# Kernel optimization log

Measured on AMD Instinct MI355X. Metric: run time of the kernel, lower is better.

The kernel has to match this reference:

```python
import jax, jax.numpy as jnp
import numpy as np

INPUT, HIDDEN, CLASSES = 4096, 4096, 1000


def setup_inputs() -> dict:
    key = jax.random.key(0)
    kx, kw1, kb1, kw2, kb2 = jax.random.split(key, 5)
    return {
        "x": jax.random.normal(kx, (8192, INPUT), dtype=jnp.float32),
        "fc1_weight": jax.random.normal(kw1, (HIDDEN, INPUT), dtype=jnp.float32),
        "fc1_bias": jax.random.normal(kb1, (HIDDEN,), dtype=jnp.float32),
        "fc2_weight": jax.random.normal(kw2, (CLASSES, HIDDEN), dtype=jnp.float32),
        "fc2_bias": jax.random.normal(kb2, (CLASSES,), dtype=jnp.float32),
    }


def reference(x, fc1_weight, fc1_bias, fc2_weight, fc2_bias):
    # x: [B, INPUT] (module flattens; already flat here)
    hidden = jnp.einsum("bi,hi->bh", x, fc1_weight) + fc1_bias  # [B, H]
    activated = jax.nn.relu(hidden)
    logits = jnp.einsum("bh,ch->bc", activated, fc2_weight) + fc2_bias  # [B, C]
    return jax.nn.softmax(logits, axis=-1)
```

## Files before the change

kernel.cpp:

```cpp
#include <hip/hip_runtime.h>
#include <hip/hip_fp16.h>
#include <stdint.h>

typedef __attribute__((ext_vector_type(8)))  _Float16 f16x8;
typedef __attribute__((ext_vector_type(4)))  _Float16 f16x4;
typedef __attribute__((ext_vector_type(4)))  float    f32x4;
typedef __attribute__((ext_vector_type(16))) float    f32x16;

__device__ __forceinline__ void split4(const f32x4 v, f16x4 &h, f16x4 &l) {
    #pragma unroll
    for (int i = 0; i < 4; ++i) {
        float a = v[i];
        _Float16 hh = (_Float16)a;
        h[i] = hh;
        l[i] = (_Float16)(a - (float)hh);
    }
}

__global__ __launch_bounds__(256)
void split_rows(const float* __restrict__ src, _Float16* __restrict__ h,
                _Float16* __restrict__ l, int srcRows, long long total4)
{
    const long long stride = (long long)gridDim.x * blockDim.x;
    for (long long i = (long long)blockIdx.x * blockDim.x + threadIdx.x; i < total4; i += stride) {
        const long long e = i << 2;
        const int row = (int)(e >> 12);
        f16x4 hv = {}, lv = {};
        if (row < srcRows) {
            f32x4 v = *(const f32x4*)(src + e);
            split4(v, hv, lv);
        }
        *(f16x4*)(h + e) = hv;
        *(f16x4*)(l + e) = lv;
    }
}


#define BARRIER() __builtin_amdgcn_s_barrier()
#define SB0()     __builtin_amdgcn_sched_barrier(0)
#define MFMA32    __builtin_amdgcn_mfma_f32_32x32x16_f16

template<int N> __device__ __forceinline__ void VMCNT() {
    asm volatile("s_waitcnt vmcnt(%0)" :: "n"(N) : "memory");
    __builtin_amdgcn_sched_barrier(0);
}

__device__ __forceinline__ void gload16(const _Float16* g, _Float16* l) {
    __builtin_amdgcn_global_load_lds(
        (const __attribute__((address_space(1))) void*)g,
        (__attribute__((address_space(3))) void*)l, 16, 0, 0);
}

template<int MI, bool SPLITOUT, bool CHUNKSWZ>
__global__ __launch_bounds__(512, 2)
void gemm3_v6(const _Float16* __restrict__ Agh, const _Float16* __restrict__ Agl,
              const _Float16* __restrict__ Bgh, const _Float16* __restrict__ Bgl,
              const float* __restrict__ bias,
              _Float16* __restrict__ Oh, _Float16* __restrict__ Ol,
              float* __restrict__ Of, int ldo, int Nstore,
              int K, int nBM)
{
    extern __shared__ _Float16 lds[];
    constexpr int WROWS = MI * 16;
    constexpr int BM    = MI * 32;
    constexpr int MB    = MI / 2;
    constexpr int MBH   = MB / 2;
    constexpr int CHA   = MI * 2;
    constexpr int PW    = (2*CHA + 32) / 8;
    constexpr int H2    = CHA / 8;
    constexpr int H1    = PW - H2;
    constexpr int ALO   = CHA * 512;
    constexpr int BHO   = 2 * CHA * 512;
    constexpr int BUFS  = 2*CHA*512 + 16384;

    const int tid  = threadIdx.x;
    const int lane = tid & 63;
    const int wave = tid >> 6;
    const int wm  = wave >> 2;
    const int wn  = wave & 3;
    const int l31 = lane & 31;
    const int lhi = lane >> 5;

    int bm, bn;
    const int orig = blockIdx.x;
    if (CHUNKSWZ) {
        bm = ((orig & 7) << 2) | ((orig >> 3) & 3);
        bn = orig >> 5;
    } else {
        const int cpx  = gridDim.x >> 3;
        const int swzb = (orig & 7) * cpx + (orig >> 3);
        bm = swzb % nBM;
        bn = swzb / nBM;
    }
    const int m0 = bm * BM;
    const int n0 = bn * 256;

    const _Float16* gptr[8];
    int loff[8];
    #pragma unroll
    for (int i = 0; i < PW; ++i) {
        int p, q;
        if (i < H2 || i >= H1) {
            const bool hi = (i >= H1);
            const int  s  = hi ? (i - H1) : i;
            const int  j  = wave * H2 + s;
            p = j / (CHA / 2);
            const int v   = j % (CHA / 2);
            const int wmq = v / (MI / 2);
            const int wi  = v % (MI / 2);
            q = wmq * MI + (hi ? MI / 2 : 0) + wi;
        } else {
            q = (i - H2) + (wave & 3) * 4;
            p = 2 + (wave >> 2);
        }
        const int row = q*16 + (lane >> 2);
        const int gc  = (lane & 3) ^ ((row >> 1) & 3);
        const _Float16* plane = (p == 0) ? Agh : (p == 1) ? Agl : (p == 2) ? Bgh : Bgl;
        const size_t grow = (size_t)((p < 2) ? m0 : n0) + row;
        gptr[i] = plane + grow * (size_t)K + gc * 8;
        loff[i] = ((p < 2) ? p * ALO : BHO + (p - 2) * 8192) + q * 512;
    }

    const int kxor = (l31 >> 1) & 3;
    int aoff[MB][2], boff[2][2];
    #pragma unroll
    for (int mb = 0; mb < MB; ++mb)
        #pragma unroll
        for (int kh = 0; kh < 2; ++kh)
            aoff[mb][kh] = (wm*WROWS + mb*32 + l31)*32 + ((kh*2 + lhi) ^ kxor)*8;
    #pragma unroll
    for (int nb = 0; nb < 2; ++nb)
        #pragma unroll
        for (int kh = 0; kh < 2; ++kh)
            boff[nb][kh] = BHO + (wn*64 + nb*32 + l31)*32 + ((kh*2 + lhi) ^ kxor)*8;

    f32x16 acc[MB][2] = {};

    #pragma unroll
    for (int i = 0; i < PW; ++i) { gload16(gptr[i], &lds[loff[i]]); gptr[i] += 32; }
    VMCNT<H2>(); BARRIER(); SB0();

#define DO_HALF(MBB, IB, IE)                                                  \
    do {                                                                      \
        _Pragma("unroll")                                                     \
        for (int i = (IB); i < (IE); ++i) {                                   \
            gload16(gptr[i], &lds[nbuf + loff[i]]); gptr[i] += 32;            \
        }                                                                     \
        SB0();                                                                \
        _Pragma("unroll")                                                     \
        for (int kh = 0; kh < 2; ++kh) {                                      \
            f16x8 ah[MBH], al[MBH];                                           \
            _Pragma("unroll")                                                 \
            for (int m2 = 0; m2 < MBH; ++m2) {                                \
                ah[m2] = *(const f16x8*)&lds[bb + aoff[(MBB) + m2][kh]];      \
                al[m2] = *(const f16x8*)&lds[bb + ALO + aoff[(MBB) + m2][kh]];\
            }                                                                 \
            __builtin_amdgcn_s_setprio(1);                                    \
            _Pragma("unroll")                                                 \
            for (int m2 = 0; m2 < MBH; ++m2) {                                \
                _Pragma("unroll")                                             \
                for (int n2 = 0; n2 < 2; ++n2) {                              \
                    acc[(MBB)+m2][n2] = MFMA32(ah[m2], bh[n2][kh], acc[(MBB)+m2][n2], 0, 0, 0); \
                    acc[(MBB)+m2][n2] = MFMA32(ah[m2], bl[n2][kh], acc[(MBB)+m2][n2], 0, 0, 0); \
                    acc[(MBB)+m2][n2] = MFMA32(al[m2], bh[n2][kh], acc[(MBB)+m2][n2], 0, 0, 0); \
                }                                                             \
            }                                                                 \
            __builtin_amdgcn_s_setprio(0);                                    \
        }                                                                     \
    } while (0)

    const int NT = K >> 5;
    int bb = 0;
    for (int t = 0; t < NT - 1; ++t) {
        const int nbuf = BUFS - bb;
        f16x8 bh[2][2], bl[2][2];
        #pragma unroll
        for (int nb = 0; nb < 2; ++nb)
            #pragma unroll
            for (int kh = 0; kh < 2; ++kh) {
                bh[nb][kh] = *(const f16x8*)&lds[bb + boff[nb][kh]];
                bl[nb][kh] = *(const f16x8*)&lds[bb + 8192 + boff[nb][kh]];
            }
        DO_HALF(0, 0, H1);
        VMCNT<H1>(); BARRIER(); SB0();
        DO_HALF(MBH, H1, PW);
        VMCNT<H2>(); BARRIER(); SB0();
        bb = nbuf;
    }
    {
        const int nbuf = bb;
        f16x8 bh[2][2], bl[2][2];
        #pragma unroll
        for (int nb = 0; nb < 2; ++nb)
            #pragma unroll
            for (int kh = 0; kh < 2; ++kh) {
                bh[nb][kh] = *(const f16x8*)&lds[bb + boff[nb][kh]];
                bl[nb][kh] = *(const f16x8*)&lds[bb + 8192 + boff[nb][kh]];
            }
        DO_HALF(0, 0, 0);
        VMCNT<0>(); BARRIER(); SB0();
        DO_HALF(MBH, 0, 0);
        (void)nbuf;
    }
#undef DO_HALF

    #pragma unroll
    for (int nb = 0; nb < 2; ++nb) {
        const int n = n0 + wn*64 + nb*32 + l31;
        if (!SPLITOUT && n >= Nstore) continue;
        const float bv = bias[n];
        #pragma unroll
        for (int mb = 0; mb < MB; ++mb) {
            #pragma unroll
            for (int r = 0; r < 16; ++r) {
                const int m = m0 + wm*WROWS + mb*32 + (r & 3) + 8*(r >> 2) + 4*lhi;
                float v = acc[mb][nb][r] + bv;
                if (SPLITOUT) {
                    v = fmaxf(v, 0.f);
                    const _Float16 hh = (_Float16)v;
                    Oh[(size_t)m * ldo + n] = hh;
                    Ol[(size_t)m * ldo + n] = (_Float16)(v - (float)hh);
                } else {
                    Of[(size_t)m * ldo + n] = v;
                }
            }
        }
    }
}

#define TILE_M 128
#define TILE_N 128
#define TILE_K 32
#define LDSK   40

template<bool RELU, bool NGUARD>
__global__ __launch_bounds__(256, 2)
void gemm_split3(const float* __restrict__ A, const float* __restrict__ B,
                 const float* __restrict__ bias, float* __restrict__ C,
                 int K, int ldc, int Nreal)
{
    __shared__ _Float16 Ah[TILE_M][LDSK];
    __shared__ _Float16 Al[TILE_M][LDSK];
    __shared__ _Float16 Bh[TILE_N][LDSK];
    __shared__ _Float16 Bl[TILE_N][LDSK];

    const int tid  = threadIdx.x;
    const int lane = tid & 63;
    const int wave = tid >> 6;
    const int wr   = wave >> 1;
    const int wc   = wave & 1;
    const int m0   = blockIdx.x * TILE_M;
    const int n0   = blockIdx.y * TILE_N;
    const int srow = tid >> 3;
    const int scol = (tid & 7) << 2;
    const int fr = lane & 15;
    const int fg = lane >> 4;

    f32x4 acc[4][4] = {};

    for (int kt = 0; kt < K; kt += TILE_K) {
        __syncthreads();
        #pragma unroll
        for (int p = 0; p < 4; ++p) {
            const int row = srow + p * 32;
            f32x4 v = *(const f32x4*)(A + (size_t)(m0 + row) * K + kt + scol);
            f16x4 hv, lv;
            split4(v, hv, lv);
            *(f16x4*)&Ah[row][scol] = hv;
            *(f16x4*)&Al[row][scol] = lv;
        }
        #pragma unroll
        for (int p = 0; p < 4; ++p) {
            const int row = srow + p * 32;
            f32x4 v = {0.f, 0.f, 0.f, 0.f};
            if (!NGUARD || (n0 + row) < Nreal)
                v = *(const f32x4*)(B + (size_t)(n0 + row) * K + kt + scol);
            f16x4 hv, lv;
            split4(v, hv, lv);
            *(f16x4*)&Bh[row][scol] = hv;
            *(f16x4*)&Bl[row][scol] = lv;
        }
        __syncthreads();

        f16x8 ah[4], al[4];
        #pragma unroll
        for (int mi = 0; mi < 4; ++mi) {
            const int r = wr * 64 + mi * 16 + fr;
            ah[mi] = *(const f16x8*)&Ah[r][fg * 8];
            al[mi] = *(const f16x8*)&Al[r][fg * 8];
        }
        #pragma unroll
        for (int ni = 0; ni < 4; ++ni) {
            const int r = wc * 64 + ni * 16 + fr;
            const f16x8 bh = *(const f16x8*)&Bh[r][fg * 8];
            const f16x8 bl = *(const f16x8*)&Bl[r][fg * 8];
            #pragma unroll
            for (int mi = 0; mi < 4; ++mi) {
                acc[mi][ni] = __builtin_amdgcn_mfma_f32_16x16x32_f16(ah[mi], bh, acc[mi][ni], 0, 0, 0);
                acc[mi][ni] = __builtin_amdgcn_mfma_f32_16x16x32_f16(ah[mi], bl, acc[mi][ni], 0, 0, 0);
                acc[mi][ni] = __builtin_amdgcn_mfma_f32_16x16x32_f16(al[mi], bh, acc[mi][ni], 0, 0, 0);
            }
        }
    }

    #pragma unroll
    for (int ni = 0; ni < 4; ++ni) {
        const int n = n0 + wc * 64 + ni * 16 + fr;
        if (NGUARD && n >= Nreal) continue;
        const float bv = bias[n];
        #pragma unroll
        for (int mi = 0; mi < 4; ++mi) {
            #pragma unroll
            for (int j = 0; j < 4; ++j) {
                const int m = m0 + wr * 64 + mi * 16 + fg * 4 + j;
                float val = acc[mi][ni][j] + bv;
                if (RELU) val = fmaxf(val, 0.f);
                C[(size_t)m * ldc + n] = val;
            }
        }
    }
}

__global__ __launch_bounds__(256)
void softmax_rows(float* __restrict__ out, int rows, int cols)
{
    const int lane = threadIdx.x & 63;
    const int row  = blockIdx.x * 4 + (threadIdx.x >> 6);
    if (row >= rows) return;
    float* p = out + (size_t)row * cols;

    float v[16];
    float mx = -3.4e38f;
    #pragma unroll
    for (int j = 0; j < 16; ++j) {
        const int c = lane + j * 64;
        v[j] = (c < cols) ? p[c] : -3.4e38f;
        mx = fmaxf(mx, v[j]);
    }
    #pragma unroll
    for (int off = 32; off > 0; off >>= 1)
        mx = fmaxf(mx, __shfl_xor(mx, off));

    float s = 0.f;
    #pragma unroll
    for (int j = 0; j < 16; ++j) {
        const int c = lane + j * 64;
        const float e = (c < cols) ? __expf(v[j] - mx) : 0.f;
        v[j] = e;
        s += e;
    }
    #pragma unroll
    for (int off = 32; off > 0; off >>= 1)
        s += __shfl_xor(s, off);

    const float inv = 1.f / s;
    #pragma unroll
    for (int j = 0; j < 16; ++j) {
        const int c = lane + j * 64;
        if (c < cols) p[c] = v[j] * inv;
    }
}

extern "C" void kernel_launch(void* const* d_in, const int* in_sizes, int n_in,
                              void* d_out, int out_size, void* d_ws, size_t ws_size,
                              hipStream_t stream)
{
    const float* x  = (const float*)d_in[0];
    const float* w1 = (const float*)d_in[1];
    const float* b1 = (const float*)d_in[2];
    const float* w2 = (const float*)d_in[3];
    const float* b2 = (const float*)d_in[4];
    float* out = (float*)d_out;

    const size_t SZ_X  = (size_t)8192 * 4096 * 2;
    const size_t SZ_W1 = (size_t)4096 * 4096 * 2;
    const size_t SZ_W2 = (size_t)1024 * 4096 * 2;

    size_t off = 0;
    auto take = [&](size_t b) { size_t o = off; off += (b + 255) & ~(size_t)255; return o; };
    const size_t o_xh  = take(SZ_X),  o_xl  = take(SZ_X);
    const size_t o_w1h = take(SZ_W1), o_w1l = take(SZ_W1);
    const size_t o_w2h = take(SZ_W2), o_w2l = take(SZ_W2);
    const size_t o_ah  = take(SZ_X),  o_al  = take(SZ_X);
    const size_t need = off;

    bool attr_ok =
        (hipFuncSetAttribute((const void*)gemm3_v6<8, true, true>,
                             hipFuncAttributeMaxDynamicSharedMemorySize, 131072) == hipSuccess) &&
        (hipFuncSetAttribute((const void*)gemm3_v6<4, false, false>,
                             hipFuncAttributeMaxDynamicSharedMemorySize, 131072) == hipSuccess);

    const dim3 blk256(256, 1, 1), blk512(512, 1, 1);

    if (attr_ok && ws_size >= need) {
        char* w = (char*)d_ws;
        _Float16 *xh  = (_Float16*)(w + o_xh),  *xl  = (_Float16*)(w + o_xl);
        _Float16 *w1h = (_Float16*)(w + o_w1h), *w1l = (_Float16*)(w + o_w1l);
        _Float16 *w2h = (_Float16*)(w + o_w2h), *w2l = (_Float16*)(w + o_w2l);
        _Float16 *ath = (_Float16*)(w + o_ah),  *atl = (_Float16*)(w + o_al);

        hipLaunchKernelGGL(split_rows, dim3(2048), blk256, 0, stream, x,  xh,  xl,  8192, (long long)8192 * 1024);
        hipLaunchKernelGGL(split_rows, dim3(2048), blk256, 0, stream, w1, w1h, w1l, 4096, (long long)4096 * 1024);
        hipLaunchKernelGGL(split_rows, dim3(1024), blk256, 0, stream, w2, w2h, w2l, 1000, (long long)1024 * 1024);

        hipLaunchKernelGGL((gemm3_v6<8, true, true>), dim3(512), blk512, 131072, stream,
                           xh, xl, w1h, w1l, b1, ath, atl, (float*)nullptr, 4096, 4096, 4096, 32);
        hipLaunchKernelGGL((gemm3_v6<4, false, false>), dim3(256), blk512, 98304, stream,
                           ath, atl, w2h, w2l, b2, (_Float16*)nullptr, (_Float16*)nullptr,
                           out, 1000, 1000, 4096, 64);
        hipLaunchKernelGGL(softmax_rows, dim3(2048), blk256, 0, stream, out, 8192, 1000);
    } else {
        float* act = (float*)d_ws;
        hipLaunchKernelGGL((gemm_split3<true, false>), dim3(64, 32), blk256, 0, stream,
                           x, w1, b1, act, 4096, 4096, 4096);
        hipLaunchKernelGGL((gemm_split3<false, true>), dim3(64, 8), blk256, 0, stream,
                           act, w2, b2, out, 4096, 1000, 1000);
        hipLaunchKernelGGL(softmax_rows, dim3(2048), blk256, 0, stream, out, 8192, 1000);
    }
}
```

Measured before the change: 1.033 ms.

## Replace split-half prefetch pipeline with single-stage double buffer and swap tile raster order

The GEMM main loop drops the two-half schedule, which used partial vmcnt waits and an extra barrier per K tile. Instead it issues all global-to-LDS loads for the next tile up front, runs every MFMA for the current tile, then waits for all loads and barriers once. The peeled last iteration goes away. The swizzle for the non-chunked path now rasterizes N-fastest using nBN, and the k-subchunk assignment for LDS reads is permuted the same way for A and B. The simpler schedule has fewer barriers but may expose more load latency, because each iteration ends with a full vmcnt(0) wait.

```diff
diff --git a/kernel.cpp b/kernel.cpp
--- a/kernel.cpp
+++ b/kernel.cpp
@@ -53,22 +53,21 @@
 
 template<int MI, bool SPLITOUT, bool CHUNKSWZ>
 __global__ __launch_bounds__(512, 2)
-void gemm3_v6(const _Float16* __restrict__ Agh, const _Float16* __restrict__ Agl,
+void gemm3_v7(const _Float16* __restrict__ Agh, const _Float16* __restrict__ Agl,
               const _Float16* __restrict__ Bgh, const _Float16* __restrict__ Bgl,
               const float* __restrict__ bias,
               _Float16* __restrict__ Oh, _Float16* __restrict__ Ol,
               float* __restrict__ Of, int ldo, int Nstore,
-              int K, int nBM)
+              int K, int nBN)
 {
     extern __shared__ _Float16 lds[];
     constexpr int WROWS = MI * 16;
     constexpr int BM    = MI * 32;
     constexpr int MB    = MI / 2;
-    constexpr int MBH   = MB / 2;
     constexpr int CHA   = MI * 2;
     constexpr int PW    = (2*CHA + 32) / 8;
+    constexpr int H1    = PW - CHA/8;
     constexpr int H2    = CHA / 8;
-    constexpr int H1    = PW - H2;
     constexpr int ALO   = CHA * 512;
     constexpr int BHO   = 2 * CHA * 512;
     constexpr int BUFS  = 2*CHA*512 + 16384;
@@ -89,8 +88,8 @@
     } else {
         const int cpx  = gridDim.x >> 3;
         const int swzb = (orig & 7) * cpx + (orig >> 3);
-        bm = swzb % nBM;
-        bn = swzb / nBM;
+        bn = swzb % nBN;
+        bm = swzb / nBN;
     }
     const int m0 = bm * BM;
     const int n0 = bn * 256;
@@ -127,86 +126,57 @@
     for (int mb = 0; mb < MB; ++mb)
         #pragma unroll
         for (int kh = 0; kh < 2; ++kh)
-            aoff[mb][kh] = (wm*WROWS + mb*32 + l31)*32 + ((kh*2 + lhi) ^ kxor)*8;
-    #pragma unroll
-    for (int nb = 0; nb < 2; ++nb)
+            aoff[mb][kh] = (wm*WROWS + mb*32 + l31)*32 + ((lhi*2 + kh) ^ kxor)*8;
+    #pragma unroll
+    for (int nb2 = 0; nb2 < 2; ++nb2)
         #pragma unroll
         for (int kh = 0; kh < 2; ++kh)
-            boff[nb][kh] = BHO + (wn*64 + nb*32 + l31)*32 + ((kh*2 + lhi) ^ kxor)*8;
+            boff[nb2][kh] = BHO + (wn*64 + nb2*32 + l31)*32 + ((lhi*2 + kh) ^ kxor)*8;
 
     f32x16 acc[MB][2] = {};
 
     #pragma unroll
     for (int i = 0; i < PW; ++i) { gload16(gptr[i], &lds[loff[i]]); gptr[i] += 32; }
-    VMCNT<H2>(); BARRIER(); SB0();
-
-#define DO_HALF(MBB, IB, IE)                                                  \
-    do {                                                                      \
-        _Pragma("unroll")                                                     \
-        for (int i = (IB); i < (IE); ++i) {                                   \
-            gload16(gptr[i], &lds[nbuf + loff[i]]); gptr[i] += 32;            \
-        }                                                                     \
-        SB0();                                                                \
-        _Pragma("unroll")                                                     \
-        for (int kh = 0; kh < 2; ++kh) {                                      \
-            f16x8 ah[MBH], al[MBH];                                           \
-            _Pragma("unroll")                                                 \
-            for (int m2 = 0; m2 < MBH; ++m2) {                                \
-                ah[m2] = *(const f16x8*)&lds[bb + aoff[(MBB) + m2][kh]];      \
-                al[m2] = *(const f16x8*)&lds[bb + ALO + aoff[(MBB) + m2][kh]];\
-            }                                                                 \
-            __builtin_amdgcn_s_setprio(1);                                    \
-            _Pragma("unroll")                                                 \
-            for (int m2 = 0; m2 < MBH; ++m2) {                                \
-                _Pragma("unroll")                                             \
-                for (int n2 = 0; n2 < 2; ++n2) {                              \
-                    acc[(MBB)+m2][n2] = MFMA32(ah[m2], bh[n2][kh], acc[(MBB)+m2][n2], 0, 0, 0); \
-                    acc[(MBB)+m2][n2] = MFMA32(ah[m2], bl[n2][kh], acc[(MBB)+m2][n2], 0, 0, 0); \
-                    acc[(MBB)+m2][n2] = MFMA32(al[m2], bh[n2][kh], acc[(MBB)+m2][n2], 0, 0, 0); \
-                }                                                             \
-            }                                                                 \
-            __builtin_amdgcn_s_setprio(0);                                    \
-        }                                                                     \
-    } while (0)
+    VMCNT<0>(); BARRIER(); SB0();
 
     const int NT = K >> 5;
     int bb = 0;
-    for (int t = 0; t < NT - 1; ++t) {
+    for (int t = 0; t < NT; ++t) {
         const int nbuf = BUFS - bb;
+        if (t < NT - 1) {
+            #pragma unroll
+            for (int i = 0; i < PW; ++i) { gload16(gptr[i], &lds[nbuf + loff[i]]); gptr[i] += 32; }
+        }
+        SB0();
         f16x8 bh[2][2], bl[2][2];
         #pragma unroll
-        for (int nb = 0; nb < 2; ++nb)
+        for (int nb2 = 0; nb2 < 2; ++nb2)
             #pragma unroll
             for (int kh = 0; kh < 2; ++kh) {
-                bh[nb][kh] = *(const f16x8*)&lds[bb + boff[nb][kh]];
-                bl[nb][kh] = *(const f16x8*)&lds[bb + 8192 + boff[nb][kh]];
-            }
-        DO_HALF(0, 0, H1);
-        VMCNT<H1>(); BARRIER(); SB0();
-        DO_HALF(MBH, H1, PW);
-        VMCNT<H2>(); BARRIER(); SB0();
+                bh[nb2][kh] = *(const f16x8*)&lds[bb + boff[nb2][kh]];
+                bl[nb2][kh] = *(const f16x8*)&lds[bb + 8192 + boff[nb2][kh]];
+            }
+        #pragma unroll
+        for (int kh = 0; kh < 2; ++kh) {
+            #pragma unroll
+            for (int mb = 0; mb < MB; ++mb) {
+                const f16x8 ah = *(const f16x8*)&lds[bb + aoff[mb][kh]];
+                const f16x8 al = *(const f16x8*)&lds[bb + ALO + aoff[mb][kh]];
+                #pragma unroll
+                for (int n2 = 0; n2 < 2; ++n2) {
+                    acc[mb][n2] = MFMA32(ah, bh[n2][kh], acc[mb][n2], 0, 0, 0);
+                    acc[mb][n2] = MFMA32(ah, bl[n2][kh], acc[mb][n2], 0, 0, 0);
+                    acc[mb][n2] = MFMA32(al, bh[n2][kh], acc[mb][n2], 0, 0, 0);
+                }
+            }
+        }
+        VMCNT<0>(); BARRIER(); SB0();
         bb = nbuf;
     }
-    {
-        const int nbuf = bb;
-        f16x8 bh[2][2], bl[2][2];
-        #pragma unroll
-        for (int nb = 0; nb < 2; ++nb)
-            #pragma unroll
-            for (int kh = 0; kh < 2; ++kh) {
-                bh[nb][kh] = *(const f16x8*)&lds[bb + boff[nb][kh]];
-                bl[nb][kh] = *(const f16x8*)&lds[bb + 8192 + boff[nb][kh]];
-            }
-        DO_HALF(0, 0, 0);
-        VMCNT<0>(); BARRIER(); SB0();
-        DO_HALF(MBH, 0, 0);
-        (void)nbuf;
-    }
-#undef DO_HALF
-
-    #pragma unroll
-    for (int nb = 0; nb < 2; ++nb) {
-        const int n = n0 + wn*64 + nb*32 + l31;
+
+    #pragma unroll
+    for (int nb2 = 0; nb2 < 2; ++nb2) {
+        const int n = n0 + wn*64 + nb2*32 + l31;
         if (!SPLITOUT && n >= Nstore) continue;
         const float bv = bias[n];
         #pragma unroll
@@ -214,7 +184,7 @@
             #pragma unroll
             for (int r = 0; r < 16; ++r) {
                 const int m = m0 + wm*WROWS + mb*32 + (r & 3) + 8*(r >> 2) + 4*lhi;
-                float v = acc[mb][nb][r] + bv;
+                float v = acc[mb][nb2][r] + bv;
                 if (SPLITOUT) {
                     v = fmaxf(v, 0.f);
                     const _Float16 hh = (_Float16)v;
@@ -385,9 +355,9 @@
     const size_t need = off;
 
     bool attr_ok =
-        (hipFuncSetAttribute((const void*)gemm3_v6<8, true, true>,
+        (hipFuncSetAttribute((const void*)gemm3_v7<8, true, true>,
                              hipFuncAttributeMaxDynamicSharedMemorySize, 131072) == hipSuccess) &&
-        (hipFuncSetAttribute((const void*)gemm3_v6<4, false, false>,
+        (hipFuncSetAttribute((const void*)gemm3_v7<4, false, false>,
                              hipFuncAttributeMaxDynamicSharedMemorySize, 131072) == hipSuccess);
 
     const dim3 blk256(256, 1, 1), blk512(512, 1, 1);
@@ -403,11 +373,11 @@
         hipLaunchKernelGGL(split_rows, dim3(2048), blk256, 0, stream, w1, w1h, w1l, 4096, (long long)4096 * 1024);
         hipLaunchKernelGGL(split_rows, dim3(1024), blk256, 0, stream, w2, w2h, w2l, 1000, (long long)1024 * 1024);
 
-        hipLaunchKernelGGL((gemm3_v6<8, true, true>), dim3(512), blk512, 131072, stream,
-                           xh, xl, w1h, w1l, b1, ath, atl, (float*)nullptr, 4096, 4096, 4096, 32);
-        hipLaunchKernelGGL((gemm3_v6<4, false, false>), dim3(256), blk512, 98304, stream,
+        hipLaunchKernelGGL((gemm3_v7<8, true, true>), dim3(512), blk512, 131072, stream,
+                           xh, xl, w1h, w1l, b1, ath, atl, (float*)nullptr, 4096, 4096, 4096, 16);
+        hipLaunchKernelGGL((gemm3_v7<4, false, false>), dim3(256), blk512, 98304, stream,
                            ath, atl, w2h, w2l, b2, (_Float16*)nullptr, (_Float16*)nullptr,
-                           out, 1000, 1000, 4096, 64);
+                           out, 1000, 1000, 4096, 4);
         hipLaunchKernelGGL(softmax_rows, dim3(2048), blk256, 0, stream, out, 8192, 1000);
     } else {
         float* act = (float*)d_ws;
```

Result: slower. 1.060 ms (+2.6%).
